# Kernel tuning notes

Hardware: AMD Instinct MI355X
Metric: run time of the kernel (lower is better)

The kernel has to match this reference:

```python
import jax, jax.numpy as jnp
import numpy as np

N = 60000      # total nodes
D = 300        # feature dim
R = 5          # num relations == num bases
E = 1_000_000  # edges
S = 25000      # last_idx_senses
G = 50000      # last_idx_globals
BATCH = 32


def setup_inputs() -> dict:
    key = jax.random.key(0)
    ks = jax.random.split(key, 12)
    x = jax.random.normal(ks[0], (N, D), dtype=jnp.float32)
    edge_index = jax.random.randint(ks[1], (2, E), 0, N, dtype=jnp.int32)
    edge_type = jax.random.randint(ks[2], (E,), 0, R, dtype=jnp.int32)
    current_node_index = jax.random.randint(ks[3], (BATCH,), 0, N, dtype=jnp.int32)
    scale = 1.0 / np.sqrt(D)
    # RGCNConv basis decomposition params (num_bases == num_relations)
    basis = jax.random.normal(ks[4], (R, D, D), dtype=jnp.float32) * scale
    comp = jax.random.normal(ks[5], (R, R), dtype=jnp.float32) * scale
    root = jax.random.normal(ks[6], (D, D), dtype=jnp.float32) * scale
    bias = jnp.zeros((D,), dtype=jnp.float32)
    # heads
    w_global = jax.random.normal(ks[7], (G - S, D), dtype=jnp.float32) * scale
    b_global = jnp.zeros((G - S,), dtype=jnp.float32)
    w_sense = jax.random.normal(ks[8], (S, D), dtype=jnp.float32) * scale
    b_sense = jnp.zeros((S,), dtype=jnp.float32)
    return {
        "x": x, "edge_index": edge_index, "edge_type": edge_type,
        "current_node_index": current_node_index,
        "basis": basis, "comp": comp, "root": root, "bias": bias,
        "w_global": w_global, "b_global": b_global,
        "w_sense": w_sense, "b_sense": b_sense,
    }


def reference(x, edge_index, edge_type, current_node_index,
              basis, comp, root, bias,
              w_global, b_global, w_sense, b_sense):
    src, dst = edge_index[0], edge_index[1]
    # Combined segment id over (dst node, relation): mean-aggregate source
    # features per (node, relation), then apply the per-relation transform
    # (mean(x_j) @ W_r == mean(x_j @ W_r); matches PyG RGCNConv aggr='mean').
    seg = dst * R + edge_type                      # [E]
    msg_sum = jax.ops.segment_sum(x[src], seg, num_segments=N * R)  # [N*R, D]
    cnt = jax.ops.segment_sum(jnp.ones((E,), jnp.float32), seg, num_segments=N * R)
    mean = msg_sum.reshape(N, R, D) / jnp.maximum(cnt.reshape(N, R, 1), 1.0)
    # basis decomposition: W_r = sum_b comp[r,b] * basis[b]
    W = jnp.einsum('rb,bij->rij', comp, basis)     # [R, D, D]
    agg = jnp.einsum('nrd,rde->ne', mean, W)       # [N, D]
    h = jax.nn.relu(agg + x @ root + bias)         # [N, D]
    hc = h[current_node_index]                     # [B, D]
    logits_global = hc @ w_global.T + b_global     # [B, G-S]
    logits_sense = hc @ w_sense.T + b_sense        # [B, S]
    return (jax.nn.log_softmax(logits_global, axis=-1),
            jax.nn.log_softmax(logits_sense, axis=-1))
```

## Files before the change

kernel.cpp:

```cpp
#include <hip/hip_runtime.h>
#include <hip/hip_bf16.h>
#include <math.h>

#define D 300
#define R 5
#define NE 1000000
#define B 32
#define NG 25000
#define NS 25000
#define NROWS 50000
#define NBLK 1563

typedef __bf16 bf16x8 __attribute__((ext_vector_type(8)));
typedef float f32x16 __attribute__((ext_vector_type(16)));


__device__ __forceinline__ void online_upd(float& m, float& s, float v) {
    if (v > m) { s = s * __expf(m - v) + 1.0f; m = v; }
    else       { s += __expf(v - m); }
}
__device__ __forceinline__ void online_merge(float& m, float& s, float om, float os) {
    float M = fmaxf(m, om);
    s = s * __expf(m - M) + os * __expf(om - M);
    m = M;
}

__global__ void zero_ws(float4* __restrict__ p) {
    int i = blockIdx.x * 256 + threadIdx.x;
    if (i < 14440) p[i] = float4{0.f, 0.f, 0.f, 0.f};
}

__global__ __launch_bounds__(256) void scan_accum(
        const int* __restrict__ ei, const int* __restrict__ et,
        const int* __restrict__ cur, const float* __restrict__ x,
        float* __restrict__ wsum, float* __restrict__ wcnt) {
    __shared__ unsigned int tbl[32];
    __shared__ int curl[B];
    __shared__ int lcnt;
    __shared__ int2 loc[64];
    int tid = threadIdx.x;
    if (tid < 32) tbl[tid] = 0u;
    if (tid == 0) lcnt = 0;
    __syncthreads();
    if (tid < B) { int c = cur[tid]; curl[tid] = c; atomicOr(&tbl[(c >> 5) & 31], 1u << (c & 31)); }
    __syncthreads();
    long base = ((long)blockIdx.x * 256 + tid) * 4;
    if (base < NE) {
        int ds4[4];
        if (base + 4 <= NE) {
            int4 d4 = *(const int4*)(ei + NE + base);
            ds4[0] = d4.x; ds4[1] = d4.y; ds4[2] = d4.z; ds4[3] = d4.w;
        } else {
            for (int k = 0; k < 4; ++k) ds4[k] = (base + k < NE) ? ei[NE + base + k] : -1;
        }
        #pragma unroll
        for (int k = 0; k < 4; ++k) {
            int dst = ds4[k];
            if (dst < 0) continue;
            if (!(tbl[(dst >> 5) & 31] & (1u << (dst & 31)))) continue;
            int e = (int)base + k;
            int r = -1, src = 0;
            for (int b = 0; b < B; ++b) {
                if (dst == curl[b]) {
                    if (r < 0) { r = et[e]; src = ei[e]; }
                    atomicAdd(&wcnt[b * R + r], 1.0f);
                    int p = atomicAdd(&lcnt, 1);
                    if (p < 64) loc[p] = int2{src, b * R + r};
                }
            }
        }
    }
    __syncthreads();
    int n = lcnt; if (n > 64) n = 64;
    for (int m = 0; m < n; ++m) {
        int2 pr = loc[m];
        const float* xs = x + (long)pr.x * D;
        float* sm = wsum + (long)pr.y * D;
        for (int t = tid; t < D; t += 256) atomicAdd(&sm[t], xs[t]);
    }
}

__global__ __launch_bounds__(320) void rgcn_hc(
        const float* __restrict__ x, const int* __restrict__ cur,
        const float* __restrict__ comp, const float* __restrict__ root,
        const float* __restrict__ basis, const float* __restrict__ wsum,
        const float* __restrict__ wcnt, float* __restrict__ hcf) {
    int kc = blockIdx.x, t = threadIdx.x;
    __shared__ float uL[800];
    __shared__ float inv[B * R];
    __shared__ float cmp[R * R];
    if (t < B * R) inv[t] = 1.0f / fmaxf(wcnt[t], 1.0f);
    if (t >= 160 && t < 160 + R * R) cmp[t - 160] = comp[t - 160];
    __syncthreads();
    int d0 = kc * 25;
    if (d0 < 300) {
        for (int i = t; i < 800; i += 320) {
            int b = i / 25, dd = i - b * 25;
            uL[i] = x[(long)cur[b] * D + d0 + dd];
        }
    } else {
        int g0 = d0 - 300;
        int bb = g0 / 300, t0 = g0 - bb * 300;
        for (int i = t; i < 800; i += 320) {
            int b = i / 25, dd = i - b * 25;
            float a = 0.f;
            #pragma unroll
            for (int r = 0; r < R; ++r)
                a = fmaf(cmp[r * R + bb] * inv[b * R + r], wsum[(long)(b * R + r) * D + t0 + dd], a);
            uL[i] = a;
        }
    }
    __syncthreads();
    if (t < D) {
        const float* Mb = (d0 < 300) ? (root + (long)d0 * D) : (basis + (long)(d0 - 300) * D);
        float acc[B] = {};
        #pragma unroll 5
        for (int i = 0; i < 25; ++i) {
            float m = Mb[(long)i * D + t];
            #pragma unroll
            for (int b = 0; b < B; ++b) acc[b] = fmaf(uL[b * 25 + i], m, acc[b]);
        }
        for (int b = 0; b < B; ++b) atomicAdd(&hcf[b * D + t], acc[b]);
    }
}

__global__ __launch_bounds__(256) void head_gemm_mfma(
    const float* __restrict__ hcf, const float* __restrict__ bias,
    const float* __restrict__ wg, const float* __restrict__ bg,
    const float* __restrict__ wsn, const float* __restrict__ bsn,
    float* __restrict__ out, float2* __restrict__ pm2) {
    __shared__ __bf16 hcbL[32 * 304];
    int tid = threadIdx.x;
    for (int i = tid; i < 32 * 304; i += 256) {
        int b = i / 304, kk = i - b * 304;
        float v = 0.f;
        if (kk < D) v = fmaxf(hcf[b * D + kk] + bias[kk], 0.f);
        hcbL[i] = (__bf16)v;
    }
    __syncthreads();
    int wid = tid >> 6, l = tid & 63, lm = l & 31, lh = l >> 5;
    int tile = blockIdx.x * 4 + wid;
    if (tile >= NBLK) return;

    bf16x8 bfrag[19];
    const __bf16* hrow = hcbL + lm * 304 + lh * 8;
    #pragma unroll
    for (int s = 0; s < 19; ++s) bfrag[s] = *(const bf16x8*)(hrow + 16 * s);

    int j0 = tile * 32;
    int row = j0 + lm; if (row >= NROWS) row = NROWS - 1;
    const float* wrow = ((row < NG) ? (wg + (long)row * D) : (wsn + (long)(row - NG) * D)) + lh * 8;

    f32x16 acc = {};
    #pragma unroll
    for (int s = 0; s < 18; ++s) {
        float4 w0 = *(const float4*)(wrow + 16 * s);
        float4 w1 = *(const float4*)(wrow + 16 * s + 4);
        bf16x8 a;
        a[0]=(__bf16)w0.x; a[1]=(__bf16)w0.y; a[2]=(__bf16)w0.z; a[3]=(__bf16)w0.w;
        a[4]=(__bf16)w1.x; a[5]=(__bf16)w1.y; a[6]=(__bf16)w1.z; a[7]=(__bf16)w1.w;
        acc = __builtin_amdgcn_mfma_f32_32x32x16_bf16(a, bfrag[s], acc, 0, 0, 0);
    }
    {
        float4 w0 = *(const float4*)(wrow + 288);
        float4 w1 = (lh == 0) ? *(const float4*)(wrow + 292) : float4{0.f, 0.f, 0.f, 0.f};
        bf16x8 a;
        a[0]=(__bf16)w0.x; a[1]=(__bf16)w0.y; a[2]=(__bf16)w0.z; a[3]=(__bf16)w0.w;
        a[4]=(__bf16)w1.x; a[5]=(__bf16)w1.y; a[6]=(__bf16)w1.z; a[7]=(__bf16)w1.w;
        acc = __builtin_amdgcn_mfma_f32_32x32x16_bf16(a, bfrag[18], acc, 0, 0, 0);
    }

    int b = lm;
    float m0 = -3.0e38f, s0 = 0.f, m1 = -3.0e38f, s1 = 0.f;
    #pragma unroll
    for (int r = 0; r < 16; ++r) {
        int j = j0 + (r & 3) + 8 * (r >> 2) + 4 * lh;
        if (j >= NROWS) continue;
        float bv = (j < NG) ? bg[j] : bsn[j - NG];
        float v = acc[r] + bv;
        float* op = (j < NG) ? (out + (long)b * NG + j)
                             : (out + (long)B * NG + (long)b * NS + (j - NG));
        *op = v;
        if (j < NG) online_upd(m0, s0, v); else online_upd(m1, s1, v);
    }
    float om0 = __shfl_xor(m0, 32), os0 = __shfl_xor(s0, 32);
    float om1 = __shfl_xor(m1, 32), os1 = __shfl_xor(s1, 32);
    online_merge(m0, s0, om0, os0);
    online_merge(m1, s1, om1, os1);
    if (lh == 0) {
        pm2[(long)b * NBLK + tile]       = float2{m0, s0};
        pm2[(long)(B + b) * NBLK + tile] = float2{m1, s1};
    }
}

__global__ __launch_bounds__(256) void lse_red(const float2* __restrict__ pm2,
                                               float* __restrict__ lse) {
    int rw = blockIdx.x, tid = threadIdx.x;
    const float2* pr = pm2 + (long)rw * NBLK;
    float m = -3.0e38f, s = 0.f;
    for (int i = tid; i < NBLK; i += 256) { float2 e = pr[i]; online_merge(m, s, e.x, e.y); }
    #pragma unroll
    for (int o = 32; o; o >>= 1) {
        float om = __shfl_xor(m, o), os = __shfl_xor(s, o);
        online_merge(m, s, om, os);
    }
    __shared__ float sm[4], ss[4];
    if ((tid & 63) == 0) { sm[tid >> 6] = m; ss[tid >> 6] = s; }
    __syncthreads();
    if (tid == 0) {
        float M = sm[0], S = ss[0];
        for (int w = 1; w < 4; ++w) online_merge(M, S, sm[w], ss[w]);
        lse[rw] = M + __logf(S);
    }
}

__global__ __launch_bounds__(256) void sub_lse(float* __restrict__ out,
                                               const float* __restrict__ lse) {
    int rw = blockIdx.x / 25, c = blockIdx.x % 25;
    float l = lse[rw];
    float4* o4 = (float4*)out + (long)rw * 6250 + c * 250;
    int tid = threadIdx.x;
    if (tid < 250) { float4 v = o4[tid]; v.x -= l; v.y -= l; v.z -= l; v.w -= l; o4[tid] = v; }
}

extern "C" void kernel_launch(void* const* d_in, const int* in_sizes, int n_in,
                              void* d_out, int out_size, void* d_ws, size_t ws_size,
                              hipStream_t stream) {
    const float* x     = (const float*)d_in[0];
    const int*   ei    = (const int*)d_in[1];
    const int*   et    = (const int*)d_in[2];
    const int*   cur   = (const int*)d_in[3];
    const float* basis = (const float*)d_in[4];
    const float* comp  = (const float*)d_in[5];
    const float* root  = (const float*)d_in[6];
    const float* bias  = (const float*)d_in[7];
    const float* wg    = (const float*)d_in[8];
    const float* bgl   = (const float*)d_in[9];
    const float* wsn   = (const float*)d_in[10];
    const float* bsn   = (const float*)d_in[11];
    float* out  = (float*)d_out;
    float* wsf  = (float*)d_ws;
    float*  wsum = wsf;
    float*  wcnt = wsf + 48000;
    float*  hcf  = wsf + 48160;
    float2* pm2  = (float2*)(wsf + 57760);
    float*  lse  = wsf + 257824;

    zero_ws<<<57, 256, 0, stream>>>((float4*)d_ws);
    scan_accum<<<977, 256, 0, stream>>>(ei, et, cur, x, wsum, wcnt);
    rgcn_hc<<<72, 320, 0, stream>>>(x, cur, comp, root, basis, wsum, wcnt, hcf);
    head_gemm_mfma<<<391, 256, 0, stream>>>(hcf, bias, wg, bgl, wsn, bsn, out, pm2);
    lse_red<<<64, 256, 0, stream>>>(pm2, lse);
    sub_lse<<<1600, 256, 0, stream>>>(out, lse);
}
```

Baseline: 73.94 us.

## Switch head GEMM to 16x16 MFMA tiles and precompute bf16 hidden in rgcn

The head GEMM now uses 16x16x32 bf16 MFMA with each wave covering 16 output rows by 16 batch rows, which doubles the number of waves and the partial-LSE entries. The bf16 conversion of the ReLU'd hidden state moves into the last-finishing rgcn_hc block, found with an atomic done counter, so head blocks no longer each rebuild it in LDS. The aim is more parallelism and occupancy in the weight-streaming GEMM and less redundant per-block prologue work. The cost is that each weight row is now read by two waves, lse_red has twice as many partials to merge, and there is a serialized tail in rgcn_hc.

```diff
diff --git a/kernel.cpp b/kernel.cpp
--- a/kernel.cpp
+++ b/kernel.cpp
@@ -9,10 +9,11 @@
 #define NG 25000
 #define NS 25000
 #define NROWS 50000
-#define NBLK 1563
+#define NT16 3125
+#define NW 6250
 
 typedef __bf16 bf16x8 __attribute__((ext_vector_type(8)));
-typedef float f32x16 __attribute__((ext_vector_type(16)));
+typedef float f32x4 __attribute__((ext_vector_type(4)));
 
 
 __device__ __forceinline__ void online_upd(float& m, float& s, float v) {
@@ -27,7 +28,7 @@
 
 __global__ void zero_ws(float4* __restrict__ p) {
     int i = blockIdx.x * 256 + threadIdx.x;
-    if (i < 14440) p[i] = float4{0.f, 0.f, 0.f, 0.f};
+    if (i < 14441) p[i] = float4{0.f, 0.f, 0.f, 0.f};
 }
 
 __global__ __launch_bounds__(256) void scan_accum(
@@ -83,12 +84,14 @@
 __global__ __launch_bounds__(320) void rgcn_hc(
         const float* __restrict__ x, const int* __restrict__ cur,
         const float* __restrict__ comp, const float* __restrict__ root,
-        const float* __restrict__ basis, const float* __restrict__ wsum,
-        const float* __restrict__ wcnt, float* __restrict__ hcf) {
+        const float* __restrict__ basis, const float* __restrict__ bias,
+        const float* __restrict__ wsum, const float* __restrict__ wcnt,
+        float* __restrict__ hcf, int* __restrict__ done, __bf16* __restrict__ hcb) {
     int kc = blockIdx.x, t = threadIdx.x;
     __shared__ float uL[800];
     __shared__ float inv[B * R];
     __shared__ float cmp[R * R];
+    __shared__ int lastFlag;
     if (t < B * R) inv[t] = 1.0f / fmaxf(wcnt[t], 1.0f);
     if (t >= 160 && t < 160 + R * R) cmp[t - 160] = comp[t - 160];
     __syncthreads();
@@ -122,60 +125,67 @@
         }
         for (int b = 0; b < B; ++b) atomicAdd(&hcf[b * D + t], acc[b]);
     }
-}
-
-__global__ __launch_bounds__(256) void head_gemm_mfma(
-    const float* __restrict__ hcf, const float* __restrict__ bias,
-    const float* __restrict__ wg, const float* __restrict__ bg,
+    __syncthreads();
+    if (t == 0) {
+        __threadfence();
+        int p = atomicAdd(done, 1);
+        lastFlag = (p == 71);
+    }
+    __syncthreads();
+    if (!lastFlag) return;
+    __threadfence();
+    for (int i = t; i < 32 * 320; i += 320) {
+        int b = i / 320, kk = i - b * 320;
+        float a = 0.f;
+        if (kk < D) a = fmaxf(atomicAdd(&hcf[b * D + kk], 0.0f) + bias[kk], 0.f);
+        hcb[i] = (__bf16)a;
+    }
+}
+
+__global__ __launch_bounds__(256, 6) void head_gemm16(
+    const __bf16* __restrict__ hcb, const float* __restrict__ wg, const float* __restrict__ bg,
     const float* __restrict__ wsn, const float* __restrict__ bsn,
     float* __restrict__ out, float2* __restrict__ pm2) {
-    __shared__ __bf16 hcbL[32 * 304];
-    int tid = threadIdx.x;
-    for (int i = tid; i < 32 * 304; i += 256) {
-        int b = i / 304, kk = i - b * 304;
-        float v = 0.f;
-        if (kk < D) v = fmaxf(hcf[b * D + kk] + bias[kk], 0.f);
-        hcbL[i] = (__bf16)v;
-    }
-    __syncthreads();
-    int wid = tid >> 6, l = tid & 63, lm = l & 31, lh = l >> 5;
-    int tile = blockIdx.x * 4 + wid;
-    if (tile >= NBLK) return;
-
-    bf16x8 bfrag[19];
-    const __bf16* hrow = hcbL + lm * 304 + lh * 8;
-    #pragma unroll
-    for (int s = 0; s < 19; ++s) bfrag[s] = *(const bf16x8*)(hrow + 16 * s);
-
-    int j0 = tile * 32;
-    int row = j0 + lm; if (row >= NROWS) row = NROWS - 1;
-    const float* wrow = ((row < NG) ? (wg + (long)row * D) : (wsn + (long)(row - NG) * D)) + lh * 8;
-
-    f32x16 acc = {};
-    #pragma unroll
-    for (int s = 0; s < 18; ++s) {
-        float4 w0 = *(const float4*)(wrow + 16 * s);
-        float4 w1 = *(const float4*)(wrow + 16 * s + 4);
+    int tid = threadIdx.x, wid = tid >> 6, l = tid & 63;
+    int gw = blockIdx.x * 4 + wid;
+    if (gw >= NW) return;
+    int jt = gw >> 1, bh = gw & 1;
+    int j0 = jt * 16;
+    int ln = l & 15, og = l >> 4;
+    int b = bh * 16 + ln;
+
+    bf16x8 bfrag[10];
+    const __bf16* hrow = hcb + b * 320 + og * 8;
+    #pragma unroll
+    for (int s = 0; s < 10; ++s) bfrag[s] = *(const bf16x8*)(hrow + 32 * s);
+
+    int row = j0 + ln;
+    const float* wrow = ((row < NG) ? (wg + (long)row * D) : (wsn + (long)(row - NG) * D)) + og * 8;
+
+    f32x4 acc = {};
+    #pragma unroll
+    for (int s = 0; s < 9; ++s) {
+        float4 w0 = *(const float4*)(wrow + 32 * s);
+        float4 w1 = *(const float4*)(wrow + 32 * s + 4);
         bf16x8 a;
         a[0]=(__bf16)w0.x; a[1]=(__bf16)w0.y; a[2]=(__bf16)w0.z; a[3]=(__bf16)w0.w;
         a[4]=(__bf16)w1.x; a[5]=(__bf16)w1.y; a[6]=(__bf16)w1.z; a[7]=(__bf16)w1.w;
-        acc = __builtin_amdgcn_mfma_f32_32x32x16_bf16(a, bfrag[s], acc, 0, 0, 0);
+        acc = __builtin_amdgcn_mfma_f32_16x16x32_bf16(a, bfrag[s], acc, 0, 0, 0);
     }
     {
-        float4 w0 = *(const float4*)(wrow + 288);
-        float4 w1 = (lh == 0) ? *(const float4*)(wrow + 292) : float4{0.f, 0.f, 0.f, 0.f};
+        float4 w0 = float4{0.f,0.f,0.f,0.f}, w1 = float4{0.f,0.f,0.f,0.f};
+        if (og == 0) { w0 = *(const float4*)(wrow + 288); w1 = *(const float4*)(wrow + 292); }
+        else if (og == 1) { w0 = *(const float4*)(wrow + 288); }
         bf16x8 a;
         a[0]=(__bf16)w0.x; a[1]=(__bf16)w0.y; a[2]=(__bf16)w0.z; a[3]=(__bf16)w0.w;
         a[4]=(__bf16)w1.x; a[5]=(__bf16)w1.y; a[6]=(__bf16)w1.z; a[7]=(__bf16)w1.w;
-        acc = __builtin_amdgcn_mfma_f32_32x32x16_bf16(a, bfrag[18], acc, 0, 0, 0);
-    }
-
-    int b = lm;
+        acc = __builtin_amdgcn_mfma_f32_16x16x32_bf16(a, bfrag[9], acc, 0, 0, 0);
+    }
+
     float m0 = -3.0e38f, s0 = 0.f, m1 = -3.0e38f, s1 = 0.f;
     #pragma unroll
-    for (int r = 0; r < 16; ++r) {
-        int j = j0 + (r & 3) + 8 * (r >> 2) + 4 * lh;
-        if (j >= NROWS) continue;
+    for (int r = 0; r < 4; ++r) {
+        int j = j0 + og * 4 + r;
         float bv = (j < NG) ? bg[j] : bsn[j - NG];
         float v = acc[r] + bv;
         float* op = (j < NG) ? (out + (long)b * NG + j)
@@ -183,22 +193,25 @@
         *op = v;
         if (j < NG) online_upd(m0, s0, v); else online_upd(m1, s1, v);
     }
-    float om0 = __shfl_xor(m0, 32), os0 = __shfl_xor(s0, 32);
-    float om1 = __shfl_xor(m1, 32), os1 = __shfl_xor(s1, 32);
-    online_merge(m0, s0, om0, os0);
-    online_merge(m1, s1, om1, os1);
-    if (lh == 0) {
-        pm2[(long)b * NBLK + tile]       = float2{m0, s0};
-        pm2[(long)(B + b) * NBLK + tile] = float2{m1, s1};
+    #pragma unroll
+    for (int o = 16; o <= 32; o <<= 1) {
+        float om0 = __shfl_xor(m0, o), os0 = __shfl_xor(s0, o);
+        float om1 = __shfl_xor(m1, o), os1 = __shfl_xor(s1, o);
+        online_merge(m0, s0, om0, os0);
+        online_merge(m1, s1, om1, os1);
+    }
+    if (og == 0) {
+        pm2[(long)b * NT16 + jt]       = float2{m0, s0};
+        pm2[(long)(B + b) * NT16 + jt] = float2{m1, s1};
     }
 }
 
 __global__ __launch_bounds__(256) void lse_red(const float2* __restrict__ pm2,
                                                float* __restrict__ lse) {
     int rw = blockIdx.x, tid = threadIdx.x;
-    const float2* pr = pm2 + (long)rw * NBLK;
+    const float2* pr = pm2 + (long)rw * NT16;
     float m = -3.0e38f, s = 0.f;
-    for (int i = tid; i < NBLK; i += 256) { float2 e = pr[i]; online_merge(m, s, e.x, e.y); }
+    for (int i = tid; i < NT16; i += 256) { float2 e = pr[i]; online_merge(m, s, e.x, e.y); }
     #pragma unroll
     for (int o = 32; o; o >>= 1) {
         float om = __shfl_xor(m, o), os = __shfl_xor(s, o);
@@ -243,13 +256,15 @@
     float*  wsum = wsf;
     float*  wcnt = wsf + 48000;
     float*  hcf  = wsf + 48160;
-    float2* pm2  = (float2*)(wsf + 57760);
-    float*  lse  = wsf + 257824;
+    int*    done = (int*)(wsf + 57760);
+    __bf16* hcb  = (__bf16*)(wsf + 57764);
+    float2* pm2  = (float2*)(wsf + 62884);
+    float*  lse  = wsf + 462884;
 
     zero_ws<<<57, 256, 0, stream>>>((float4*)d_ws);
     scan_accum<<<977, 256, 0, stream>>>(ei, et, cur, x, wsum, wcnt);
-    rgcn_hc<<<72, 320, 0, stream>>>(x, cur, comp, root, basis, wsum, wcnt, hcf);
-    head_gemm_mfma<<<391, 256, 0, stream>>>(hcf, bias, wg, bgl, wsn, bsn, out, pm2);
+    rgcn_hc<<<72, 320, 0, stream>>>(x, cur, comp, root, basis, bias, wsum, wcnt, hcf, done, hcb);
+    head_gemm16<<<(NW + 3) / 4, 256, 0, stream>>>(hcb, wg, bgl, wsn, bsn, out, pm2);
     lse_red<<<64, 256, 0, stream>>>(pm2, lse);
     sub_lse<<<1600, 256, 0, stream>>>(out, lse);
 }
```

After: 81.61 us. 10.4% more time.
